# Kernel optimization log

Measured on AMD Instinct MI355X. Metric: run time of the kernel, lower is better.

The kernel has to match this reference:

```python
import jax, jax.numpy as jnp
import numpy as np

T, S, B, E, H, FF = 1024, 1024, 4, 1024, 16, 4096
DH = E // H
EPS = 1e-5


def layer_norm(x, g, b):
    mu = jnp.mean(x, axis=-1, keepdims=True)
    var = jnp.mean(jnp.square(x - mu), axis=-1, keepdims=True)
    return (x - mu) * jax.lax.rsqrt(var + EPS) * g + b


def mha(q_in, k_in, v_in, wq, bq, wk, bk, wv, bv, wo, bo, attn_mask=None):
    # q_in: [T,B,E]; k_in/v_in: [S,B,E]; torch Linear: x @ W.T + b
    Tq = q_in.shape[0]
    q = (q_in @ wq.T + bq).reshape(Tq, B, H, DH)
    k = (k_in @ wk.T + bk).reshape(-1, B, H, DH)
    v = (v_in @ wv.T + bv).reshape(-1, B, H, DH)
    scores = jnp.einsum('tbhd,sbhd->bhts', q, k) / np.sqrt(DH).astype(np.float32)
    if attn_mask is not None:
        scores = scores + attn_mask  # broadcast [T,S] over [B,H,T,S]
    w = jax.nn.softmax(scores, axis=-1)
    attn = jnp.einsum('bhts,sbhd->tbhd', w, v).reshape(Tq, B, E)
    return attn @ wo.T + bo, w


def setup_inputs() -> dict:
    key = jax.random.key(0)
    ks = jax.random.split(key, 32)
    def W(k, o, i):
        return (jax.random.normal(k, (o, i), jnp.float32) * (1.0 / np.sqrt(i))).astype(jnp.float32)
    d = {}
    d['state'] = jax.random.normal(ks[0], (T, B, E), jnp.float32)
    d['encoder_out'] = jax.random.normal(ks[1], (S, B, E), jnp.float32)
    causal = jnp.where(jnp.arange(T)[:, None] >= jnp.arange(T)[None, :], 0.0, -1e9).astype(jnp.float32)
    d['self_attn_mask'] = causal
    names = ['sa_wq', 'sa_wk', 'sa_wv', 'sa_wo', 'ea_wq', 'ea_wk', 'ea_wv', 'ea_wo']
    for i, n in enumerate(names):
        d[n] = W(ks[2 + i], E, E)
        d[n.replace('w', 'b')] = jnp.zeros((E,), jnp.float32)
    d['fc1_w'] = W(ks[10], FF, E)
    d['fc1_b'] = jnp.zeros((FF,), jnp.float32)
    d['fc2_w'] = W(ks[11], E, FF)
    d['fc2_b'] = jnp.zeros((E,), jnp.float32)
    for i, n in enumerate(['ln1', 'ln2', 'ln3']):
        d[n + '_g'] = 1.0 + 0.02 * jax.random.normal(ks[12 + i], (E,), jnp.float32)
        d[n + '_b'] = 0.02 * jax.random.normal(ks[15 + i], (E,), jnp.float32)
    return d


def reference(state, encoder_out, self_attn_mask,
              sa_wq, sa_bq, sa_wk, sa_bk, sa_wv, sa_bv, sa_wo, sa_bo,
              ea_wq, ea_bq, ea_wk, ea_bk, ea_wv, ea_bv, ea_wo, ea_bo,
              fc1_w, fc1_b, fc2_w, fc2_b,
              ln1_g, ln1_b, ln2_g, ln2_b, ln3_g, ln3_b):
    # self-attention block (dropout p applied in eval mode -> identity)
    residual = state
    x, _ = mha(state, state, state, sa_wq, sa_bq, sa_wk, sa_bk, sa_wv, sa_bv, sa_wo, sa_bo, self_attn_mask)
    state = layer_norm(x + residual, ln1_g, ln1_b)
    # encoder-decoder attention
    residual = state
    x, attn_w = mha(state, encoder_out, encoder_out, ea_wq, ea_bq, ea_wk, ea_bk, ea_wv, ea_bv, ea_wo, ea_bo, None)
    state = layer_norm(x + residual, ln2_g, ln2_b)
    # FFN
    residual = state
    x = jax.nn.relu(state @ fc1_w.T + fc1_b)
    x = x @ fc2_w.T + fc2_b
    state = layer_norm(x + residual, ln3_g, ln3_b)
    return state, attn_w
```

## Files before the change

kernel.cpp:

```cpp
#include <hip/hip_runtime.h>
#include <stdint.h>

typedef __bf16 bf16;
typedef __bf16 bf16x4 __attribute__((ext_vector_type(4)));
typedef __bf16 bf16x8 __attribute__((ext_vector_type(8)));
typedef float f32x4 __attribute__((ext_vector_type(4)));

#define LOG2E 1.44269504088896340736f

__device__ __forceinline__ void gload16(const void* g, void* l) {
  __builtin_amdgcn_global_load_lds(
      (const __attribute__((address_space(1))) void*)g,
      (__attribute__((address_space(3))) void*)l, 16, 0, 0);
}

__global__ void detect_dtype(const uint32_t* __restrict__ mask, int* __restrict__ flag) {
  if (threadIdx.x == 0 && blockIdx.x == 0)
    *flag = (mask[0] == 0xCE6E0000u) ? 1 : 0;
}

__device__ __forceinline__ bf16x8 ld8(const void* p, int64_t idx, bool isb) {
  if (isb) {
    return *(const bf16x8*)((const bf16*)p + idx);
  } else {
    const float* f = (const float*)p + idx;
    const f32x4 a = *(const f32x4*)f;
    const f32x4 b = *(const f32x4*)(f + 4);
    bf16x8 r;
#pragma unroll
    for (int i = 0; i < 4; ++i) { r[i] = (bf16)a[i]; r[4 + i] = (bf16)b[i]; }
    return r;
  }
}

__device__ __forceinline__ float ld1(const void* p, int64_t idx, bool isb) {
  return isb ? (float)((const bf16*)p + idx)[0] : ((const float*)p + idx)[0];
}

__global__ __launch_bounds__(256)
void cvt_bf16(const void* __restrict__ src, bf16* __restrict__ dst,
              const int n8, const int* __restrict__ dflag) {
  const bool isb = (*dflag != 0);
  const int i = blockIdx.x * 256 + threadIdx.x;
  if (i < n8) *(bf16x8*)(dst + (int64_t)i * 8) = ld8(src, (int64_t)i * 8, isb);
}

__global__ __launch_bounds__(256)
void cvt3_bf16(const void* __restrict__ s0, const void* __restrict__ s1,
               const void* __restrict__ s2, bf16* __restrict__ dst,
               const int* __restrict__ dflag) {
  const bool isb = (*dflag != 0);
  const int i = blockIdx.x * 256 + threadIdx.x;
  const int sel = i >> 17;
  const int j = i & 131071;
  const void* s = (sel == 0) ? s0 : (sel == 1) ? s1 : s2;
  *(bf16x8*)(dst + (int64_t)i * 8) = ld8(s, (int64_t)j * 8, isb);
}

template <bool RELU>
__global__ __launch_bounds__(256, 4)
void gemm128(const bf16* __restrict__ A, const bf16* __restrict__ W,
             const void* __restrict__ bias, bf16* __restrict__ C,
             const int N, const int K, const int* __restrict__ dflag) {
  const bool isb = (*dflag != 0);
  __shared__ bf16 As[2][4096];
  __shared__ bf16 Bs[2][4096];
  const int tid = threadIdx.x;
  const int lane = tid & 63;
  const int wv = tid >> 6;
  const int wm = (wv >> 1) * 64;
  const int wn = (wv & 1) * 64;
  const int qd = lane >> 4;
  const int r = lane & 15;
  const int m0 = blockIdx.y * 128;
  const int n0 = blockIdx.x * 128;

  f32x4 acc[4][4] = {};
  const int c0 = tid, c1 = 256 + tid;
  const int rowA0 = c0 >> 2, colA0 = (c0 & 3) * 8;
  const int rowA1 = c1 >> 2, colA1 = (c1 & 3) * 8;
  const bf16* Ab = A + (int64_t)m0 * K;
  const bf16* Wb = W + (int64_t)n0 * K;
  const int lb0 = wv * 512, lb1 = 2048 + wv * 512;

#define STAGE_G(b, kt) do {                                        \
    gload16(&Ab[(int64_t)rowA0 * K + (kt) + colA0], &As[b][lb0]);  \
    gload16(&Ab[(int64_t)rowA1 * K + (kt) + colA1], &As[b][lb1]);  \
    gload16(&Wb[(int64_t)rowA0 * K + (kt) + colA0], &Bs[b][lb0]);  \
    gload16(&Wb[(int64_t)rowA1 * K + (kt) + colA1], &Bs[b][lb1]);  \
  } while (0)

  STAGE_G(0, 0);
  __syncthreads();
  int cur = 0;
  for (int k0 = 0; k0 < K; k0 += 32) {
    if (k0 + 32 < K) STAGE_G(cur ^ 1, k0 + 32);
    bf16x8 af[4], bfr[4];
#pragma unroll
    for (int i = 0; i < 4; ++i)
      af[i] = *(const bf16x8*)&As[cur][(wm + i * 16 + r) * 32 + qd * 8];
#pragma unroll
    for (int j = 0; j < 4; ++j)
      bfr[j] = *(const bf16x8*)&Bs[cur][(wn + j * 16 + r) * 32 + qd * 8];
#pragma unroll
    for (int i = 0; i < 4; ++i)
#pragma unroll
      for (int j = 0; j < 4; ++j)
        acc[i][j] = __builtin_amdgcn_mfma_f32_16x16x32_bf16(af[i], bfr[j], acc[i][j], 0, 0, 0);
    __syncthreads();
    cur ^= 1;
  }
#undef STAGE_G

#pragma unroll
  for (int i = 0; i < 4; ++i) {
    const int mbase = m0 + wm + i * 16 + qd * 4;
#pragma unroll
    for (int j = 0; j < 4; ++j) {
      const int n = n0 + wn + j * 16 + r;
      const float bv = ld1(bias, n, isb);
#pragma unroll
      for (int rr = 0; rr < 4; ++rr) {
        float v = acc[i][j][rr] + bv;
        if (RELU) v = fmaxf(v, 0.f);
        C[(int64_t)(mbase + rr) * N + n] = (bf16)v;
      }
    }
  }
}

__global__ __launch_bounds__(256, 4)
void gemm64(const bf16* __restrict__ A, const bf16* __restrict__ W,
            const void* __restrict__ bias, bf16* __restrict__ C,
            const int N, const int K, const int* __restrict__ dflag) {
  const bool isb = (*dflag != 0);
  __shared__ bf16 As[2][4096];
  __shared__ bf16 Bs[2][2048];
  const int tid = threadIdx.x;
  const int lane = tid & 63;
  const int wv = tid >> 6;
  const int wm = wv * 32;
  const int qd = lane >> 4;
  const int r = lane & 15;
  const int m0 = blockIdx.y * 128;
  const int n0 = blockIdx.x * 64;

  f32x4 acc[2][4] = {};
  const int c0 = tid, c1 = 256 + tid;
  const int rowA0 = c0 >> 2, colA0 = (c0 & 3) * 8;
  const int rowA1 = c1 >> 2, colA1 = (c1 & 3) * 8;
  const int rowB = tid >> 2, colB = (tid & 3) * 8;
  const bf16* Ab = A + (int64_t)m0 * K;
  const bf16* Wb = W + (int64_t)n0 * K;
  const int lb0 = wv * 512, lb1 = 2048 + wv * 512;

#define STAGE_G64(b, kt) do {                                      \
    gload16(&Ab[(int64_t)rowA0 * K + (kt) + colA0], &As[b][lb0]);  \
    gload16(&Ab[(int64_t)rowA1 * K + (kt) + colA1], &As[b][lb1]);  \
    gload16(&Wb[(int64_t)rowB * K + (kt) + colB], &Bs[b][lb0]);    \
  } while (0)

  STAGE_G64(0, 0);
  __syncthreads();
  int cur = 0;
  for (int k0 = 0; k0 < K; k0 += 32) {
    if (k0 + 32 < K) STAGE_G64(cur ^ 1, k0 + 32);
    bf16x8 af[2], bfr[4];
#pragma unroll
    for (int i = 0; i < 2; ++i)
      af[i] = *(const bf16x8*)&As[cur][(wm + i * 16 + r) * 32 + qd * 8];
#pragma unroll
    for (int j = 0; j < 4; ++j)
      bfr[j] = *(const bf16x8*)&Bs[cur][(j * 16 + r) * 32 + qd * 8];
#pragma unroll
    for (int i = 0; i < 2; ++i)
#pragma unroll
      for (int j = 0; j < 4; ++j)
        acc[i][j] = __builtin_amdgcn_mfma_f32_16x16x32_bf16(af[i], bfr[j], acc[i][j], 0, 0, 0);
    __syncthreads();
    cur ^= 1;
  }
#undef STAGE_G64

#pragma unroll
  for (int i = 0; i < 2; ++i) {
    const int mbase = m0 + wm + i * 16 + qd * 4;
#pragma unroll
    for (int j = 0; j < 4; ++j) {
      const int n = n0 + j * 16 + r;
      const float bv = ld1(bias, n, isb);
#pragma unroll
      for (int rr = 0; rr < 4; ++rr)
        C[(int64_t)(mbase + rr) * N + n] = (bf16)(acc[i][j][rr] + bv);
    }
  }
}

__global__ __launch_bounds__(256, 4)
void gemm_qkv(const bf16* __restrict__ A0, const bf16* __restrict__ A1,
              const bf16* __restrict__ W,
              const void* __restrict__ Bq, const void* __restrict__ Bk,
              const void* __restrict__ Bv,
              bf16* __restrict__ Qo, bf16* __restrict__ Ko, bf16* __restrict__ Vo,
              const int* __restrict__ dflag) {
  const bool isb = (*dflag != 0);
  const int K = 1024;
  __shared__ bf16 As[2][4096];
  __shared__ bf16 Bs[2][4096];
  const int tid = threadIdx.x;
  const int lane = tid & 63;
  const int wv = tid >> 6;
  const int wm = (wv >> 1) * 64;
  const int wn = (wv & 1) * 64;
  const int qd = lane >> 4;
  const int r = lane & 15;
  const int m0 = blockIdx.y * 128;
  const int n0 = blockIdx.x * 128;
  const int sel = n0 >> 10;
  const bf16* A = sel ? A1 : A0;
  const void* bias = (sel == 0) ? Bq : (sel == 1) ? Bk : Bv;

  f32x4 acc[4][4] = {};
  const int c0 = tid, c1 = 256 + tid;
  const int rowA0 = c0 >> 2, colA0 = (c0 & 3) * 8;
  const int rowA1 = c1 >> 2, colA1 = (c1 & 3) * 8;
  const bf16* Ab = A + (int64_t)m0 * K;
  const bf16* Wb = W + (int64_t)n0 * K;
  const int lb0 = wv * 512, lb1 = 2048 + wv * 512;

#define STAGE_GQ(b, kt) do {                                       \
    gload16(&Ab[(int64_t)rowA0 * K + (kt) + colA0], &As[b][lb0]);  \
    gload16(&Ab[(int64_t)rowA1 * K + (kt) + colA1], &As[b][lb1]);  \
    gload16(&Wb[(int64_t)rowA0 * K + (kt) + colA0], &Bs[b][lb0]);  \
    gload16(&Wb[(int64_t)rowA1 * K + (kt) + colA1], &Bs[b][lb1]);  \
  } while (0)

  STAGE_GQ(0, 0);
  __syncthreads();
  int cur = 0;
  for (int k0 = 0; k0 < K; k0 += 32) {
    if (k0 + 32 < K) STAGE_GQ(cur ^ 1, k0 + 32);
    bf16x8 af[4], bfr[4];
#pragma unroll
    for (int i = 0; i < 4; ++i)
      af[i] = *(const bf16x8*)&As[cur][(wm + i * 16 + r) * 32 + qd * 8];
#pragma unroll
    for (int j = 0; j < 4; ++j)
      bfr[j] = *(const bf16x8*)&Bs[cur][(wn + j * 16 + r) * 32 + qd * 8];
#pragma unroll
    for (int i = 0; i < 4; ++i)
#pragma unroll
      for (int j = 0; j < 4; ++j)
        acc[i][j] = __builtin_amdgcn_mfma_f32_16x16x32_bf16(af[i], bfr[j], acc[i][j], 0, 0, 0);
    __syncthreads();
    cur ^= 1;
  }
#undef STAGE_GQ

  bf16* Cq = (sel == 0) ? Qo : Ko;
#pragma unroll
  for (int i = 0; i < 4; ++i) {
    const int mbase = m0 + wm + i * 16 + qd * 4;
#pragma unroll
    for (int j = 0; j < 4; ++j) {
      const int nl = (n0 & 1023) + wn + j * 16 + r;
      const int h = nl >> 6, d = nl & 63;
      const float bv = ld1(bias, nl, isb);
#pragma unroll
      for (int rr = 0; rr < 4; ++rr) {
        const float v = acc[i][j][rr] + bv;
        const int m = mbase + rr;
        const int t = m >> 2, b = m & 3;
        if (sel < 2) {
          Cq[(((int64_t)(b * 16 + h)) * 1024 + t) * 64 + d] = (bf16)v;
        } else {
          Vo[(((int64_t)(b * 16 + h)) * 64 + d) * 1024 + t] = (bf16)v;
        }
      }
    }
  }
}

template <bool CAUSAL, bool POUT>
__global__ __launch_bounds__(256, 4)
void attn_fused(const bf16* __restrict__ Q, const bf16* __restrict__ Kt,
                const bf16* __restrict__ VT, bf16* __restrict__ O,
                void* __restrict__ dout, const int* __restrict__ dflag) {
  const bool isb = POUT ? (*dflag != 0) : false;
  const int lane = threadIdx.x & 63;
  const int wv   = threadIdx.x >> 6;
  const int bh   = blockIdx.y;
  const int tq0  = blockIdx.x * 64 + wv * 16;
  const int qd   = lane >> 4;
  const int r    = lane & 15;
  const int t    = tq0 + r;
  const bf16* Qb = Q  + (int64_t)bh * 65536;
  const bf16* Kb = Kt + (int64_t)bh * 65536;
  const bf16* Vb = VT + (int64_t)bh * 65536;
  bf16*  PoutB = POUT ? ((bf16*)dout + 4194304) : nullptr;
  float* PoutF = POUT ? ((float*)dout + 4194304) : nullptr;

  __shared__ bf16 Pl[4][16 * 40];
  bf16* myP = Pl[wv];

  const bf16x8 aq0 = *(const bf16x8*)&Qb[t * 64 + qd * 8];
  const bf16x8 aq1 = *(const bf16x8*)&Qb[t * 64 + 32 + qd * 8];

  const int nchunk = CAUSAL ? ((tq0 + 47) >> 5) : 32;
  const float SC2 = 0.125f * LOG2E;
  const float NEG = -1e30f;

  float m = NEG, l = 0.f;

  for (int c = 0; c < nchunk; ++c) {
    const int s0 = c * 32;
    f32x4 sc0 = {}, sc1 = {};
    const bf16x8 k0a = *(const bf16x8*)&Kb[(s0 + r) * 64 + qd * 8];
    const bf16x8 k0b = *(const bf16x8*)&Kb[(s0 + r) * 64 + 32 + qd * 8];
    const bf16x8 k1a = *(const bf16x8*)&Kb[(s0 + 16 + r) * 64 + qd * 8];
    const bf16x8 k1b = *(const bf16x8*)&Kb[(s0 + 16 + r) * 64 + 32 + qd * 8];
    sc0 = __builtin_amdgcn_mfma_f32_16x16x32_bf16(k0a, aq0, sc0, 0, 0, 0);
    sc0 = __builtin_amdgcn_mfma_f32_16x16x32_bf16(k0b, aq1, sc0, 0, 0, 0);
    sc1 = __builtin_amdgcn_mfma_f32_16x16x32_bf16(k1a, aq0, sc1, 0, 0, 0);
    sc1 = __builtin_amdgcn_mfma_f32_16x16x32_bf16(k1b, aq1, sc1, 0, 0, 0);
    const int sb = s0 + qd * 4;
    float v[8];
#pragma unroll
    for (int rr = 0; rr < 4; ++rr) {
      v[rr]     = (CAUSAL && (sb + rr > t))      ? NEG : sc0[rr] * SC2;
      v[4 + rr] = (CAUSAL && (sb + 16 + rr > t)) ? NEG : sc1[rr] * SC2;
    }
    const float cmax = fmaxf(fmaxf(fmaxf(v[0], v[1]), fmaxf(v[2], v[3])),
                             fmaxf(fmaxf(v[4], v[5]), fmaxf(v[6], v[7])));
    if (POUT) {
      const float nm = fmaxf(m, cmax);
      float add = 0.f;
#pragma unroll
      for (int i = 0; i < 8; ++i) add += exp2f(v[i] - nm);
      l = l * exp2f(m - nm) + add;
      m = nm;
    } else {
      m = fmaxf(m, cmax);
    }
  }
#pragma unroll
  for (int off = 16; off < 64; off <<= 1) {
    const float mo = __shfl_xor(m, off, 64);
    if (POUT) {
      const float lo = __shfl_xor(l, off, 64);
      const float nm = fmaxf(m, mo);
      l = l * exp2f(m - nm) + lo * exp2f(mo - nm);
      m = nm;
    } else {
      m = fmaxf(m, mo);
    }
  }
  const float inv = POUT ? (1.f / l) : 0.f;
  if (!POUT) l = 0.f;

  f32x4 oacc[4] = {};

  for (int c = 0; c < nchunk; ++c) {
    const int s0 = c * 32;
    f32x4 sc0 = {}, sc1 = {};
    const bf16x8 k0a = *(const bf16x8*)&Kb[(s0 + r) * 64 + qd * 8];
    const bf16x8 k0b = *(const bf16x8*)&Kb[(s0 + r) * 64 + 32 + qd * 8];
    const bf16x8 k1a = *(const bf16x8*)&Kb[(s0 + 16 + r) * 64 + qd * 8];
    const bf16x8 k1b = *(const bf16x8*)&Kb[(s0 + 16 + r) * 64 + 32 + qd * 8];
    sc0 = __builtin_amdgcn_mfma_f32_16x16x32_bf16(k0a, aq0, sc0, 0, 0, 0);
    sc0 = __builtin_amdgcn_mfma_f32_16x16x32_bf16(k0b, aq1, sc0, 0, 0, 0);
    sc1 = __builtin_amdgcn_mfma_f32_16x16x32_bf16(k1a, aq0, sc1, 0, 0, 0);
    sc1 = __builtin_amdgcn_mfma_f32_16x16x32_bf16(k1b, aq1, sc1, 0, 0, 0);
    const int sb = s0 + qd * 4;
    f32x4 P0, P1;
    bf16x4 q0, q1;
#pragma unroll
    for (int rr = 0; rr < 4; ++rr) {
      float v0 = (CAUSAL && (sb + rr > t))      ? NEG : sc0[rr] * SC2;
      float v1 = (CAUSAL && (sb + 16 + rr > t)) ? NEG : sc1[rr] * SC2;
      float p0 = exp2f(v0 - m);
      float p1 = exp2f(v1 - m);
      if (POUT) { p0 *= inv; p1 *= inv; }
      else      { l += p0 + p1; }
      P0[rr] = p0; P1[rr] = p1;
      q0[rr] = (bf16)p0; q1[rr] = (bf16)p1;
    }
    *(bf16x4*)&myP[r * 40 + qd * 4]      = q0;
    *(bf16x4*)&myP[r * 40 + 16 + qd * 4] = q1;
    if (POUT) {
      const int64_t pi = ((int64_t)bh * 1024 + t) * 1024 + sb;
      if (isb) {
        __builtin_nontemporal_store(q0, (bf16x4*)(PoutB + pi));
        __builtin_nontemporal_store(q1, (bf16x4*)(PoutB + pi + 16));
      } else {
        __builtin_nontemporal_store(P0, (f32x4*)(PoutF + pi));
        __builtin_nontemporal_store(P1, (f32x4*)(PoutF + pi + 16));
      }
    }
    const bf16x8 ap = *(const bf16x8*)&myP[r * 40 + qd * 8];
#pragma unroll
    for (int dt = 0; dt < 4; ++dt) {
      const bf16x8 bv = *(const bf16x8*)&Vb[(dt * 16 + r) * 1024 + s0 + qd * 8];
      oacc[dt] = __builtin_amdgcn_mfma_f32_16x16x32_bf16(ap, bv, oacc[dt], 0, 0, 0);
    }
  }

  if (!POUT) {
#pragma unroll
    for (int off = 16; off < 64; off <<= 1)
      l += __shfl_xor(l, off, 64);
  }

  const int b = bh >> 4, h = bh & 15;
#pragma unroll
  for (int dt = 0; dt < 4; ++dt)
#pragma unroll
    for (int rr = 0; rr < 4; ++rr) {
      const int tq = tq0 + qd * 4 + rr;
      float ov = oacc[dt][rr];
      if (!POUT) ov /= __shfl(l, qd * 4 + rr, 64);
      O[(int64_t)(tq * 4 + b) * 1024 + h * 64 + dt * 16 + r] = (bf16)ov;
    }
}

__global__ __launch_bounds__(256)
void ln_kernel(const bf16* __restrict__ x, const void* __restrict__ res,
               const void* __restrict__ g, const void* __restrict__ bta,
               void* __restrict__ out, const int res_ext, const int out_ext,
               const int* __restrict__ dflag) {
  const bool isb  = (*dflag != 0);
  const bool resb = res_ext ? isb : true;
  const bool outb = out_ext ? isb : true;
  const int row = blockIdx.x;
  const int tid = threadIdx.x;
  const bf16* xr = x + (int64_t)row * 1024;
  const int64_t rbase = (int64_t)row * 1024;
  float v[4];
  float s = 0.f, s2 = 0.f;
#pragma unroll
  for (int i = 0; i < 4; ++i) {
    const int e = tid + i * 256;
    v[i] = (float)xr[e] + ld1(res, rbase + e, resb);
    s += v[i];
    s2 += v[i] * v[i];
  }
#pragma unroll
  for (int off = 32; off > 0; off >>= 1) {
    s += __shfl_xor(s, off, 64);
    s2 += __shfl_xor(s2, off, 64);
  }
  __shared__ float red[8];
  const int wv = tid >> 6, lane = tid & 63;
  if (lane == 0) { red[wv] = s; red[4 + wv] = s2; }
  __syncthreads();
  s  = red[0] + red[1] + red[2] + red[3];
  s2 = red[4] + red[5] + red[6] + red[7];
  const float mu  = s * (1.f / 1024.f);
  const float var = s2 * (1.f / 1024.f) - mu * mu;
  const float rs  = rsqrtf(var + 1e-5f);
#pragma unroll
  for (int i = 0; i < 4; ++i) {
    const int e = tid + i * 256;
    const float o = (v[i] - mu) * rs * ld1(g, e, isb) + ld1(bta, e, isb);
    if (outb) ((bf16*)out)[rbase + e] = (bf16)o;
    else      ((float*)out)[rbase + e] = o;
  }
}

extern "C" void kernel_launch(void* const* d_in, const int* in_sizes, int n_in,
                              void* d_out, int out_size, void* d_ws, size_t ws_size,
                              hipStream_t stream) {
  (void)in_sizes; (void)n_in; (void)out_size; (void)ws_size;
  const void* state = d_in[0];
  const void* enc   = d_in[1];
  const void* mask  = d_in[2];
  const void* sa_wq = d_in[3];  const void* sa_bq = d_in[4];
  const void* sa_wk = d_in[5];  const void* sa_bk = d_in[6];
  const void* sa_wv = d_in[7];  const void* sa_bv = d_in[8];
  const void* sa_wo = d_in[9];  const void* sa_bo = d_in[10];
  const void* ea_wq = d_in[11]; const void* ea_bq = d_in[12];
  const void* ea_wk = d_in[13]; const void* ea_bk = d_in[14];
  const void* ea_wv = d_in[15]; const void* ea_bv = d_in[16];
  const void* ea_wo = d_in[17]; const void* ea_bo = d_in[18];
  const void* fc1_w = d_in[19]; const void* fc1_b = d_in[20];
  const void* fc2_w = d_in[21]; const void* fc2_b = d_in[22];
  const void* ln1_g = d_in[23]; const void* ln1_b = d_in[24];
  const void* ln2_g = d_in[25]; const void* ln2_b = d_in[26];
  const void* ln3_g = d_in[27]; const void* ln3_b = d_in[28];

  const int64_t SZ = 4LL * 1024 * 1024;
  bf16* R0 = (bf16*)d_ws;
  bf16* R1 = R0 + SZ;
  bf16* R2 = R1 + SZ;
  bf16* R3 = R2 + SZ;
  bf16* R4 = R3 + SZ;
  bf16* R5 = R4 + SZ;
  int* dflag = (int*)(R5 + SZ);
  const int64_t W3 = 3LL * 1024 * 1024;

  dim3 blk(256, 1, 1);

  detect_dtype<<<1, 64, 0, stream>>>((const uint32_t*)mask, dflag);

  cvt3_bf16<<<1536, blk, 0, stream>>>(sa_wq, sa_wk, sa_wv, R3, dflag);
  cvt_bf16<<<512,  blk, 0, stream>>>(sa_wo, R3 + W3, 131072, dflag);
  cvt_bf16<<<2048, blk, 0, stream>>>(state, R4, 524288, dflag);
  gemm_qkv<<<dim3(24, 32), blk, 0, stream>>>(R4, R4, R3, sa_bq, sa_bk, sa_bv,
                                             R0, R1, R2, dflag);
  attn_fused<true, false><<<dim3(16, 64), blk, 0, stream>>>(R0, R1, R2, R4, nullptr, dflag);
  gemm64<<<dim3(16, 32), blk, 0, stream>>>(R4, R3 + W3, sa_bo, R0, 1024, 1024, dflag);
  ln_kernel<<<4096, blk, 0, stream>>>(R0, state, ln1_g, ln1_b, R5, 1, 0, dflag);

  cvt3_bf16<<<1536, blk, 0, stream>>>(ea_wq, ea_wk, ea_wv, R3, dflag);
  cvt_bf16<<<512,  blk, 0, stream>>>(ea_wo, R3 + W3, 131072, dflag);
  cvt_bf16<<<2048, blk, 0, stream>>>(enc, R4, 524288, dflag);
  gemm_qkv<<<dim3(24, 32), blk, 0, stream>>>(R5, R4, R3, ea_bq, ea_bk, ea_bv,
                                             R0, R1, R2, dflag);
  attn_fused<false, true><<<dim3(16, 64), blk, 0, stream>>>(R0, R1, R2, R4, d_out, dflag);
  gemm64<<<dim3(16, 32), blk, 0, stream>>>(R4, R3 + W3, ea_bo, R0, 1024, 1024, dflag);
  ln_kernel<<<4096, blk, 0, stream>>>(R0, R5, ln2_g, ln2_b, R1, 0, 0, dflag);

  cvt_bf16<<<2048, blk, 0, stream>>>(fc1_w, R0, 524288, dflag);
  gemm128<true><<<dim3(32, 32), blk, 0, stream>>>(R1, R0, fc1_b, R2, 4096, 1024, dflag);
  cvt_bf16<<<2048, blk, 0, stream>>>(fc2_w, (bf16*)d_out, 524288, dflag);
  gemm64<<<dim3(16, 32), blk, 0, stream>>>(R2, (const bf16*)d_out, fc2_b, R0, 1024, 4096, dflag);
  ln_kernel<<<4096, blk, 0, stream>>>(R0, R1, ln3_g, ln3_b, d_out, 0, 1, dflag);
}
```

Measured before the change: 990.4 us.

## Double query rows per attention wave, add XCD block swizzle, merge weight converts

The attention kernel now gives each wave 32 query rows instead of 16, so every K and V fragment loaded from global memory feeds twice as many MFMAs. It launches a flat 1D grid whose block index is remapped so neighbouring heads land on the same XCD. The GEMM kernels get an XCD-aware block swizzle aimed at better L2 locality. The four projection-weight conversions are merged into one launch. In exchange, register pressure in attention roughly doubles (launch bounds lowered to 2 blocks per CU), and causal load balance per block becomes coarser.

Result: faster. 856.2 us (-13.6%).

```diff
diff --git a/kernel.cpp b/kernel.cpp
--- a/kernel.cpp
+++ b/kernel.cpp
@@ -12,6 +12,15 @@
   __builtin_amdgcn_global_load_lds(
       (const __attribute__((address_space(1))) void*)g,
       (__attribute__((address_space(3))) void*)l, 16, 0, 0);
+}
+
+__device__ __forceinline__ void xcd_swz(int& tx, int& ty) {
+  const int nx = gridDim.x;
+  const int bid = blockIdx.y * nx + blockIdx.x;
+  const int i = bid >> 3;
+  const int iy = i / nx;
+  tx = i - iy * nx;
+  ty = (bid & 7) * (gridDim.y >> 3) + iy;
 }
 
 __global__ void detect_dtype(const uint32_t* __restrict__ mask, int* __restrict__ flag) {
@@ -46,14 +55,14 @@
 }
 
 __global__ __launch_bounds__(256)
-void cvt3_bf16(const void* __restrict__ s0, const void* __restrict__ s1,
-               const void* __restrict__ s2, bf16* __restrict__ dst,
-               const int* __restrict__ dflag) {
+void cvt4_bf16(const void* __restrict__ s0, const void* __restrict__ s1,
+               const void* __restrict__ s2, const void* __restrict__ s3,
+               bf16* __restrict__ dst, const int* __restrict__ dflag) {
   const bool isb = (*dflag != 0);
   const int i = blockIdx.x * 256 + threadIdx.x;
   const int sel = i >> 17;
   const int j = i & 131071;
-  const void* s = (sel == 0) ? s0 : (sel == 1) ? s1 : s2;
+  const void* s = (sel == 0) ? s0 : (sel == 1) ? s1 : (sel == 2) ? s2 : s3;
   *(bf16x8*)(dst + (int64_t)i * 8) = ld8(s, (int64_t)j * 8, isb);
 }
 
@@ -72,8 +81,10 @@
   const int wn = (wv & 1) * 64;
   const int qd = lane >> 4;
   const int r = lane & 15;
-  const int m0 = blockIdx.y * 128;
-  const int n0 = blockIdx.x * 128;
+  int tx, ty;
+  xcd_swz(tx, ty);
+  const int m0 = ty * 128;
+  const int n0 = tx * 128;
 
   f32x4 acc[4][4] = {};
   const int c0 = tid, c1 = 256 + tid;
@@ -142,8 +153,10 @@
   const int wm = wv * 32;
   const int qd = lane >> 4;
   const int r = lane & 15;
-  const int m0 = blockIdx.y * 128;
-  const int n0 = blockIdx.x * 64;
+  int tx, ty;
+  xcd_swz(tx, ty);
+  const int m0 = ty * 128;
+  const int n0 = tx * 64;
 
   f32x4 acc[2][4] = {};
   const int c0 = tid, c1 = 256 + tid;
@@ -214,8 +227,10 @@
   const int wn = (wv & 1) * 64;
   const int qd = lane >> 4;
   const int r = lane & 15;
-  const int m0 = blockIdx.y * 128;
-  const int n0 = blockIdx.x * 128;
+  int tx, ty;
+  xcd_swz(tx, ty);
+  const int m0 = ty * 128;
+  const int n0 = tx * 128;
   const int sel = n0 >> 10;
   const bf16* A = sel ? A1 : A0;
   const void* bias = (sel == 0) ? Bq : (sel == 1) ? Bk : Bv;
@@ -282,133 +297,163 @@
 }
 
 template <bool CAUSAL, bool POUT>
-__global__ __launch_bounds__(256, 4)
+__global__ __launch_bounds__(256, 2)
 void attn_fused(const bf16* __restrict__ Q, const bf16* __restrict__ Kt,
                 const bf16* __restrict__ VT, bf16* __restrict__ O,
                 void* __restrict__ dout, const int* __restrict__ dflag) {
   const bool isb = POUT ? (*dflag != 0) : false;
   const int lane = threadIdx.x & 63;
   const int wv   = threadIdx.x >> 6;
-  const int bh   = blockIdx.y;
-  const int tq0  = blockIdx.x * 64 + wv * 16;
+  const int bid  = blockIdx.x;
+  const int i5   = bid >> 3;
+  const int bh   = (bid & 7) * 8 + (i5 >> 3);
+  const int tq0  = (i5 & 7) * 128 + wv * 32;
   const int qd   = lane >> 4;
   const int r    = lane & 15;
-  const int t    = tq0 + r;
+  const int t0   = tq0 + r;
+  const int t1   = tq0 + 16 + r;
   const bf16* Qb = Q  + (int64_t)bh * 65536;
   const bf16* Kb = Kt + (int64_t)bh * 65536;
   const bf16* Vb = VT + (int64_t)bh * 65536;
   bf16*  PoutB = POUT ? ((bf16*)dout + 4194304) : nullptr;
   float* PoutF = POUT ? ((float*)dout + 4194304) : nullptr;
 
-  __shared__ bf16 Pl[4][16 * 40];
+  __shared__ bf16 Pl[4][32 * 40];
   bf16* myP = Pl[wv];
 
-  const bf16x8 aq0 = *(const bf16x8*)&Qb[t * 64 + qd * 8];
-  const bf16x8 aq1 = *(const bf16x8*)&Qb[t * 64 + 32 + qd * 8];
-
-  const int nchunk = CAUSAL ? ((tq0 + 47) >> 5) : 32;
+  const bf16x8 aq0 = *(const bf16x8*)&Qb[t0 * 64 + qd * 8];
+  const bf16x8 aq1 = *(const bf16x8*)&Qb[t0 * 64 + 32 + qd * 8];
+  const bf16x8 aq2 = *(const bf16x8*)&Qb[t1 * 64 + qd * 8];
+  const bf16x8 aq3 = *(const bf16x8*)&Qb[t1 * 64 + 32 + qd * 8];
+
+  const int nchunk = CAUSAL ? ((tq0 >> 5) + 1) : 32;
   const float SC2 = 0.125f * LOG2E;
   const float NEG = -1e30f;
 
-  float m = NEG, l = 0.f;
+  float m0 = NEG, m1 = NEG, l0 = 0.f, l1 = 0.f;
+
+#define QK_MFMA                                                           \
+    const bf16x8 k0a = *(const bf16x8*)&Kb[(s0 + r) * 64 + qd * 8];       \
+    const bf16x8 k0b = *(const bf16x8*)&Kb[(s0 + r) * 64 + 32 + qd * 8];  \
+    const bf16x8 k1a = *(const bf16x8*)&Kb[(s0 + 16 + r) * 64 + qd * 8];  \
+    const bf16x8 k1b = *(const bf16x8*)&Kb[(s0 + 16 + r) * 64 + 32 + qd * 8]; \
+    f32x4 scA0 = {}, scA1 = {}, scB0 = {}, scB1 = {};                     \
+    scA0 = __builtin_amdgcn_mfma_f32_16x16x32_bf16(k0a, aq0, scA0, 0, 0, 0); \
+    scA0 = __builtin_amdgcn_mfma_f32_16x16x32_bf16(k0b, aq1, scA0, 0, 0, 0); \
+    scA1 = __builtin_amdgcn_mfma_f32_16x16x32_bf16(k1a, aq0, scA1, 0, 0, 0); \
+    scA1 = __builtin_amdgcn_mfma_f32_16x16x32_bf16(k1b, aq1, scA1, 0, 0, 0); \
+    scB0 = __builtin_amdgcn_mfma_f32_16x16x32_bf16(k0a, aq2, scB0, 0, 0, 0); \
+    scB0 = __builtin_amdgcn_mfma_f32_16x16x32_bf16(k0b, aq3, scB0, 0, 0, 0); \
+    scB1 = __builtin_amdgcn_mfma_f32_16x16x32_bf16(k1a, aq2, scB1, 0, 0, 0); \
+    scB1 = __builtin_amdgcn_mfma_f32_16x16x32_bf16(k1b, aq3, scB1, 0, 0, 0)
 
   for (int c = 0; c < nchunk; ++c) {
     const int s0 = c * 32;
-    f32x4 sc0 = {}, sc1 = {};
-    const bf16x8 k0a = *(const bf16x8*)&Kb[(s0 + r) * 64 + qd * 8];
-    const bf16x8 k0b = *(const bf16x8*)&Kb[(s0 + r) * 64 + 32 + qd * 8];
-    const bf16x8 k1a = *(const bf16x8*)&Kb[(s0 + 16 + r) * 64 + qd * 8];
-    const bf16x8 k1b = *(const bf16x8*)&Kb[(s0 + 16 + r) * 64 + 32 + qd * 8];
-    sc0 = __builtin_amdgcn_mfma_f32_16x16x32_bf16(k0a, aq0, sc0, 0, 0, 0);
-    sc0 = __builtin_amdgcn_mfma_f32_16x16x32_bf16(k0b, aq1, sc0, 0, 0, 0);
-    sc1 = __builtin_amdgcn_mfma_f32_16x16x32_bf16(k1a, aq0, sc1, 0, 0, 0);
-    sc1 = __builtin_amdgcn_mfma_f32_16x16x32_bf16(k1b, aq1, sc1, 0, 0, 0);
+    QK_MFMA;
     const int sb = s0 + qd * 4;
-    float v[8];
+    float vA[8], vB[8];
 #pragma unroll
     for (int rr = 0; rr < 4; ++rr) {
-      v[rr]     = (CAUSAL && (sb + rr > t))      ? NEG : sc0[rr] * SC2;
-      v[4 + rr] = (CAUSAL && (sb + 16 + rr > t)) ? NEG : sc1[rr] * SC2;
-    }
-    const float cmax = fmaxf(fmaxf(fmaxf(v[0], v[1]), fmaxf(v[2], v[3])),
-                             fmaxf(fmaxf(v[4], v[5]), fmaxf(v[6], v[7])));
+      vA[rr]     = (CAUSAL && (sb + rr > t0))      ? NEG : scA0[rr] * SC2;
+      vA[4 + rr] = (CAUSAL && (sb + 16 + rr > t0)) ? NEG : scA1[rr] * SC2;
+      vB[rr]     = (CAUSAL && (sb + rr > t1))      ? NEG : scB0[rr] * SC2;
+      vB[4 + rr] = (CAUSAL && (sb + 16 + rr > t1)) ? NEG : scB1[rr] * SC2;
+    }
+    const float cmA = fmaxf(fmaxf(fmaxf(vA[0], vA[1]), fmaxf(vA[2], vA[3])),
+                            fmaxf(fmaxf(vA[4], vA[5]), fmaxf(vA[6], vA[7])));
+    const float cmB = fmaxf(fmaxf(fmaxf(vB[0], vB[1]), fmaxf(vB[2], vB[3])),
+                            fmaxf(fmaxf(vB[4], vB[5]), fmaxf(vB[6], vB[7])));
     if (POUT) {
-      const float nm = fmaxf(m, cmax);
-      float add = 0.f;
-#pragma unroll
-      for (int i = 0; i < 8; ++i) add += exp2f(v[i] - nm);
-      l = l * exp2f(m - nm) + add;
-      m = nm;
+      const float nmA = fmaxf(m0, cmA);
+      const float nmB = fmaxf(m1, cmB);
+      float addA = 0.f, addB = 0.f;
+#pragma unroll
+      for (int i = 0; i < 8; ++i) { addA += exp2f(vA[i] - nmA); addB += exp2f(vB[i] - nmB); }
+      l0 = l0 * exp2f(m0 - nmA) + addA;  m0 = nmA;
+      l1 = l1 * exp2f(m1 - nmB) + addB;  m1 = nmB;
     } else {
-      m = fmaxf(m, cmax);
+      m0 = fmaxf(m0, cmA);
+      m1 = fmaxf(m1, cmB);
     }
   }
 #pragma unroll
   for (int off = 16; off < 64; off <<= 1) {
-    const float mo = __shfl_xor(m, off, 64);
+    const float moA = __shfl_xor(m0, off, 64);
+    const float moB = __shfl_xor(m1, off, 64);
     if (POUT) {
-      const float lo = __shfl_xor(l, off, 64);
-      const float nm = fmaxf(m, mo);
-      l = l * exp2f(m - nm) + lo * exp2f(mo - nm);
-      m = nm;
+      const float loA = __shfl_xor(l0, off, 64);
+      const float loB = __shfl_xor(l1, off, 64);
+      const float nmA = fmaxf(m0, moA);
+      const float nmB = fmaxf(m1, moB);
+      l0 = l0 * exp2f(m0 - nmA) + loA * exp2f(moA - nmA);  m0 = nmA;
+      l1 = l1 * exp2f(m1 - nmB) + loB * exp2f(moB - nmB);  m1 = nmB;
     } else {
-      m = fmaxf(m, mo);
-    }
-  }
-  const float inv = POUT ? (1.f / l) : 0.f;
-  if (!POUT) l = 0.f;
-
-  f32x4 oacc[4] = {};
+      m0 = fmaxf(m0, moA);
+      m1 = fmaxf(m1, moB);
+    }
+  }
+  const float inv0 = POUT ? (1.f / l0) : 0.f;
+  const float inv1 = POUT ? (1.f / l1) : 0.f;
+  if (!POUT) { l0 = 0.f; l1 = 0.f; }
+
+  f32x4 oaccA[4] = {}, oaccB[4] = {};
 
   for (int c = 0; c < nchunk; ++c) {
     const int s0 = c * 32;
-    f32x4 sc0 = {}, sc1 = {};
-    const bf16x8 k0a = *(const bf16x8*)&Kb[(s0 + r) * 64 + qd * 8];
-    const bf16x8 k0b = *(const bf16x8*)&Kb[(s0 + r) * 64 + 32 + qd * 8];
-    const bf16x8 k1a = *(const bf16x8*)&Kb[(s0 + 16 + r) * 64 + qd * 8];
-    const bf16x8 k1b = *(const bf16x8*)&Kb[(s0 + 16 + r) * 64 + 32 + qd * 8];
-    sc0 = __builtin_amdgcn_mfma_f32_16x16x32_bf16(k0a, aq0, sc0, 0, 0, 0);
-    sc0 = __builtin_amdgcn_mfma_f32_16x16x32_bf16(k0b, aq1, sc0, 0, 0, 0);
-    sc1 = __builtin_amdgcn_mfma_f32_16x16x32_bf16(k1a, aq0, sc1, 0, 0, 0);
-    sc1 = __builtin_amdgcn_mfma_f32_16x16x32_bf16(k1b, aq1, sc1, 0, 0, 0);
+    QK_MFMA;
     const int sb = s0 + qd * 4;
-    f32x4 P0, P1;
-    bf16x4 q0, q1;
+    f32x4 PA0, PA1, PB0, PB1;
+    bf16x4 qA0, qA1, qB0, qB1;
 #pragma unroll
     for (int rr = 0; rr < 4; ++rr) {
-      float v0 = (CAUSAL && (sb + rr > t))      ? NEG : sc0[rr] * SC2;
-      float v1 = (CAUSAL && (sb + 16 + rr > t)) ? NEG : sc1[rr] * SC2;
-      float p0 = exp2f(v0 - m);
-      float p1 = exp2f(v1 - m);
-      if (POUT) { p0 *= inv; p1 *= inv; }
-      else      { l += p0 + p1; }
-      P0[rr] = p0; P1[rr] = p1;
-      q0[rr] = (bf16)p0; q1[rr] = (bf16)p1;
-    }
-    *(bf16x4*)&myP[r * 40 + qd * 4]      = q0;
-    *(bf16x4*)&myP[r * 40 + 16 + qd * 4] = q1;
+      float vA0 = (CAUSAL && (sb + rr > t0))      ? NEG : scA0[rr] * SC2;
+      float vA1 = (CAUSAL && (sb + 16 + rr > t0)) ? NEG : scA1[rr] * SC2;
+      float vB0 = (CAUSAL && (sb + rr > t1))      ? NEG : scB0[rr] * SC2;
+      float vB1 = (CAUSAL && (sb + 16 + rr > t1)) ? NEG : scB1[rr] * SC2;
+      float pA0 = exp2f(vA0 - m0), pA1 = exp2f(vA1 - m0);
+      float pB0 = exp2f(vB0 - m1), pB1 = exp2f(vB1 - m1);
+      if (POUT) { pA0 *= inv0; pA1 *= inv0; pB0 *= inv1; pB1 *= inv1; }
+      else      { l0 += pA0 + pA1; l1 += pB0 + pB1; }
+      PA0[rr] = pA0; PA1[rr] = pA1; PB0[rr] = pB0; PB1[rr] = pB1;
+      qA0[rr] = (bf16)pA0; qA1[rr] = (bf16)pA1;
+      qB0[rr] = (bf16)pB0; qB1[rr] = (bf16)pB1;
+    }
+    *(bf16x4*)&myP[r * 40 + qd * 4]             = qA0;
+    *(bf16x4*)&myP[r * 40 + 16 + qd * 4]        = qA1;
+    *(bf16x4*)&myP[(16 + r) * 40 + qd * 4]      = qB0;
+    *(bf16x4*)&myP[(16 + r) * 40 + 16 + qd * 4] = qB1;
     if (POUT) {
-      const int64_t pi = ((int64_t)bh * 1024 + t) * 1024 + sb;
+      const int64_t piA = ((int64_t)bh * 1024 + t0) * 1024 + sb;
+      const int64_t piB = ((int64_t)bh * 1024 + t1) * 1024 + sb;
       if (isb) {
-        __builtin_nontemporal_store(q0, (bf16x4*)(PoutB + pi));
-        __builtin_nontemporal_store(q1, (bf16x4*)(PoutB + pi + 16));
+        __builtin_nontemporal_store(qA0, (bf16x4*)(PoutB + piA));
+        __builtin_nontemporal_store(qA1, (bf16x4*)(PoutB + piA + 16));
+        __builtin_nontemporal_store(qB0, (bf16x4*)(PoutB + piB));
+        __builtin_nontemporal_store(qB1, (bf16x4*)(PoutB + piB + 16));
       } else {
-        __builtin_nontemporal_store(P0, (f32x4*)(PoutF + pi));
-        __builtin_nontemporal_store(P1, (f32x4*)(PoutF + pi + 16));
+        __builtin_nontemporal_store(PA0, (f32x4*)(PoutF + piA));
+        __builtin_nontemporal_store(PA1, (f32x4*)(PoutF + piA + 16));
+        __builtin_nontemporal_store(PB0, (f32x4*)(PoutF + piB));
+        __builtin_nontemporal_store(PB1, (f32x4*)(PoutF + piB + 16));
       }
     }
-    const bf16x8 ap = *(const bf16x8*)&myP[r * 40 + qd * 8];
+    const bf16x8 apA = *(const bf16x8*)&myP[r * 40 + qd * 8];
+    const bf16x8 apB = *(const bf16x8*)&myP[(16 + r) * 40 + qd * 8];
 #pragma unroll
     for (int dt = 0; dt < 4; ++dt) {
       const bf16x8 bv = *(const bf16x8*)&Vb[(dt * 16 + r) * 1024 + s0 + qd * 8];
-      oacc[dt] = __builtin_amdgcn_mfma_f32_16x16x32_bf16(ap, bv, oacc[dt], 0, 0, 0);
-    }
-  }
+      oaccA[dt] = __builtin_amdgcn_mfma_f32_16x16x32_bf16(apA, bv, oaccA[dt], 0, 0, 0);
+      oaccB[dt] = __builtin_amdgcn_mfma_f32_16x16x32_bf16(apB, bv, oaccB[dt], 0, 0, 0);
+    }
+  }
+#undef QK_MFMA
 
   if (!POUT) {
 #pragma unroll
-    for (int off = 16; off < 64; off <<= 1)
-      l += __shfl_xor(l, off, 64);
+    for (int off = 16; off < 64; off <<= 1) {
+      l0 += __shfl_xor(l0, off, 64);
+      l1 += __shfl_xor(l1, off, 64);
+    }
   }
 
   const int b = bh >> 4, h = bh & 15;
@@ -416,10 +461,15 @@
   for (int dt = 0; dt < 4; ++dt)
 #pragma unroll
     for (int rr = 0; rr < 4; ++rr) {
-      const int tq = tq0 + qd * 4 + rr;
-      float ov = oacc[dt][rr];
-      if (!POUT) ov /= __shfl(l, qd * 4 + rr, 64);
-      O[(int64_t)(tq * 4 + b) * 1024 + h * 64 + dt * 16 + r] = (bf16)ov;
+      const int q = qd * 4 + rr;
+      float ovA = oaccA[dt][rr];
+      float ovB = oaccB[dt][rr];
+      if (!POUT) {
+        ovA /= __shfl(l0, q, 64);
+        ovB /= __shfl(l1, q, 64);
+      }
+      O[(int64_t)((tq0 + q) * 4 + b) * 1024 + h * 64 + dt * 16 + r]      = (bf16)ovA;
+      O[(int64_t)((tq0 + 16 + q) * 4 + b) * 1024 + h * 64 + dt * 16 + r] = (bf16)ovB;
     }
 }
 
@@ -502,21 +552,19 @@
 
   detect_dtype<<<1, 64, 0, stream>>>((const uint32_t*)mask, dflag);
 
-  cvt3_bf16<<<1536, blk, 0, stream>>>(sa_wq, sa_wk, sa_wv, R3, dflag);
-  cvt_bf16<<<512,  blk, 0, stream>>>(sa_wo, R3 + W3, 131072, dflag);
+  cvt4_bf16<<<2048, blk, 0, stream>>>(sa_wq, sa_wk, sa_wv, sa_wo, R3, dflag);
   cvt_bf16<<<2048, blk, 0, stream>>>(state, R4, 524288, dflag);
   gemm_qkv<<<dim3(24, 32), blk, 0, stream>>>(R4, R4, R3, sa_bq, sa_bk, sa_bv,
                                              R0, R1, R2, dflag);
-  attn_fused<true, false><<<dim3(16, 64), blk, 0, stream>>>(R0, R1, R2, R4, nullptr, dflag);
+  attn_fused<true, false><<<512, blk, 0, stream>>>(R0, R1, R2, R4, nullptr, dflag);
   gemm64<<<dim3(16, 32), blk, 0, stream>>>(R4, R3 + W3, sa_bo, R0, 1024, 1024, dflag);
   ln_kernel<<<4096, blk, 0, stream>>>(R0, state, ln1_g, ln1_b, R5, 1, 0, dflag);
 
-  cvt3_bf16<<<1536, blk, 0, stream>>>(ea_wq, ea_wk, ea_wv, R3, dflag);
-  cvt_bf16<<<512,  blk, 0, stream>>>(ea_wo, R3 + W3, 131072, dflag);
+  cvt4_bf16<<<2048, blk, 0, stream>>>(ea_wq, ea_wk, ea_wv, ea_wo, R3, dflag);
   cvt_bf16<<<2048, blk, 0, stream>>>(enc, R4, 524288, dflag);
   gemm_qkv<<<dim3(24, 32), blk, 0, stream>>>(R5, R4, R3, ea_bq, ea_bk, ea_bv,
                                              R0, R1, R2, dflag);
-  attn_fused<false, true><<<dim3(16, 64), blk, 0, stream>>>(R0, R1, R2, R4, d_out, dflag);
+  attn_fused<false, true><<<512, blk, 0, stream>>>(R0, R1, R2, R4, d_out, dflag);
   gemm64<<<dim3(16, 32), blk, 0, stream>>>(R4, R3 + W3, ea_bo, R0, 1024, 1024, dflag);
   ln_kernel<<<4096, blk, 0, stream>>>(R0, R5, ln2_g, ln2_b, R1, 0, 0, dflag);
 
```
